# Kernel tuning notes

Measured on AMD Instinct MI355X. Metric: run time of the kernel, lower is better.

Reference implementation:

```python
import jax, jax.numpy as jnp
import numpy as np

N_NODES = 10000
D_IN = 128
D_OUT = 128
N_EDGES = 640000


def setup_inputs() -> dict:
    key = jax.random.key(0)
    k_x, k_e, k_wl, k_wr, k_b = jax.random.split(key, 5)
    x = jax.random.normal(k_x, (N_NODES, D_IN), dtype=jnp.float32)
    edge_index = jax.random.randint(k_e, (2, N_EDGES), 0, N_NODES, dtype=jnp.int64)
    # SAGEConv params: lin_l (neighbor path, with bias), lin_r (root path, no bias)
    s_l = 1.0 / np.sqrt(D_IN)
    W_l = jax.random.uniform(k_wl, (D_OUT, D_IN), dtype=jnp.float32, minval=-s_l, maxval=s_l)
    b_l = jax.random.uniform(k_b, (D_OUT,), dtype=jnp.float32, minval=-s_l, maxval=s_l)
    W_r = jax.random.uniform(k_wr, (D_OUT, D_IN), dtype=jnp.float32, minval=-s_l, maxval=s_l)
    return {"x": x, "edge_index": edge_index, "W_l": W_l, "b_l": b_l, "W_r": W_r}


def reference(x, edge_index, W_l, b_l, W_r):
    x = x.astype(jnp.float32)
    src, dst = edge_index[0], edge_index[1]
    # gather source features, mean-aggregate into destination nodes
    msgs = x[src]                                   # [E, D_in] irregular gather
    agg_sum = jax.ops.segment_sum(msgs, dst, num_segments=N_NODES)  # [N, D_in]
    deg = jax.ops.segment_sum(jnp.ones((src.shape[0],), dtype=x.dtype), dst,
                              num_segments=N_NODES)                 # [N]
    agg = jnp.where(deg[:, None] > 0, agg_sum / jnp.maximum(deg, 1.0)[:, None], 0.0)
    # SAGEConv: lin_l(agg) + lin_r(x)
    y = agg @ W_l.T + b_l + x @ W_r.T               # [N, D_out]
    return x + y                                     # residual add
```

## Files before the change

### kernel.cpp

```cpp
#include <hip/hip_runtime.h>

#define N_NODES 10000
#define D 128
#define N_EDGES 640000
#define NB 128
#define EPB (N_EDGES / NB)
#define SB 40
#define NPSB 250

typedef __attribute__((ext_vector_type(8))) short bf16x8;
typedef __attribute__((ext_vector_type(4))) float f32x4;
typedef __attribute__((ext_vector_type(8))) unsigned short us8;
typedef __attribute__((ext_vector_type(8))) float f32x8;


__device__ __forceinline__ unsigned short f2bf(float f) {
    union { float f; unsigned int i; } v;
    v.f = f;
    unsigned int b = v.i;
    unsigned int rounded = b + 0x7fffu + ((b >> 16) & 1u);
    return (unsigned short)(rounded >> 16);
}

__device__ __forceinline__ float bf2f(unsigned short u) {
    union { unsigned int i; float f; } v;
    v.i = ((unsigned int)u) << 16;
    return v.f;
}

__device__ __forceinline__ f32x8 bf2f8(us8 v) {
    f32x8 r;
#pragma unroll
    for (int t = 0; t < 8; ++t) r[t] = bf2f(v[t]);
    return r;
}


__global__ __launch_bounds__(1024) void hist_cast_kernel(const int* __restrict__ ei,
                                                         const float4* __restrict__ x4,
                                                         const float4* __restrict__ Wl4,
                                                         const float4* __restrict__ Wr4,
                                                         ushort4* __restrict__ xh4,
                                                         ushort4* __restrict__ Wlb4,
                                                         ushort4* __restrict__ Wrb4,
                                                         unsigned short* __restrict__ lrank,
                                                         unsigned short* __restrict__ cnt,
                                                         unsigned long long* __restrict__ flags) {
    __shared__ int h[N_NODES];
    for (int n = threadIdx.x; n < N_NODES; n += 1024) h[n] = 0;
    if (blockIdx.x == 0 && threadIdx.x < SB) flags[threadIdx.x] = 0ULL;

    const int gid = blockIdx.x * 1024 + threadIdx.x;
    for (int i = gid; i < N_NODES * D / 4; i += NB * 1024) {
        float4 v = x4[i];
        ushort4 o;
        o.x = f2bf(v.x); o.y = f2bf(v.y); o.z = f2bf(v.z); o.w = f2bf(v.w);
        xh4[i] = o;
    }
    if (gid < D * D / 4) {
        float4 a = Wl4[gid], b = Wr4[gid];
        ushort4 oa, ob;
        oa.x = f2bf(a.x); oa.y = f2bf(a.y); oa.z = f2bf(a.z); oa.w = f2bf(a.w);
        ob.x = f2bf(b.x); ob.y = f2bf(b.y); ob.z = f2bf(b.z); ob.w = f2bf(b.w);
        Wlb4[gid] = oa;
        Wrb4[gid] = ob;
    }
    __syncthreads();

    const int base = blockIdx.x * EPB;
    for (int e = base + threadIdx.x; e < base + EPB; e += 1024) {
        int d = ei[N_EDGES + e];
        lrank[e] = (unsigned short)atomicAdd(&h[d], 1);
    }
    __syncthreads();
    unsigned short* c = cnt + (size_t)blockIdx.x * N_NODES;
    for (int n = threadIdx.x; n < N_NODES; n += 1024) c[n] = (unsigned short)h[n];
}


__global__ __launch_bounds__(256) void colscan_scan_kernel(unsigned short* __restrict__ cnt,
                                                           int* __restrict__ row_start,
                                                           unsigned long long* __restrict__ flags) {
    const int t = threadIdx.x;
    const int b = blockIdx.x;
    const int n = b * NPSB + t;
    __shared__ int sc[256];
    __shared__ int blk_excl_sh;

    int deg = 0;
    if (t < NPSB) {
        int s = 0;
#pragma unroll 8
        for (int j = 0; j < NB; ++j) {
            int idx = j * N_NODES + n;
            int v = cnt[idx];
            cnt[idx] = (unsigned short)s;
            s += v;
        }
        deg = s;
    }
    sc[t] = deg;
    __syncthreads();
    for (int off = 1; off < 256; off <<= 1) {
        int v = (t >= off) ? sc[t - off] : 0;
        __syncthreads();
        sc[t] += v;
        __syncthreads();
    }
    const int total = sc[255];
    const int local_excl = sc[t] - deg;

    if (t == 0) {
        int excl = 0;
        if (b == 0) {
            __hip_atomic_store(&flags[0], (2ULL << 32) | (unsigned)total,
                               __ATOMIC_RELEASE, __HIP_MEMORY_SCOPE_AGENT);
        } else {
            __hip_atomic_store(&flags[b], (1ULL << 32) | (unsigned)total,
                               __ATOMIC_RELEASE, __HIP_MEMORY_SCOPE_AGENT);
            int j = b - 1;
            while (j >= 0) {
                unsigned long long f = __hip_atomic_load(&flags[j], __ATOMIC_ACQUIRE,
                                                         __HIP_MEMORY_SCOPE_AGENT);
                unsigned st = (unsigned)(f >> 32);
                if (st == 0) continue;
                excl += (int)(unsigned)(f & 0xffffffffULL);
                if (st == 2) break;
                --j;
            }
            __hip_atomic_store(&flags[b], (2ULL << 32) | (unsigned)(excl + total),
                               __ATOMIC_RELEASE, __HIP_MEMORY_SCOPE_AGENT);
        }
        blk_excl_sh = excl;
    }
    __syncthreads();
    if (t < NPSB) row_start[n] = blk_excl_sh + local_excl;
    if (b == SB - 1 && t == 0) row_start[N_NODES] = N_EDGES;
}

__global__ __launch_bounds__(256) void scatter_kernel(const int* __restrict__ ei,
                                                      const int* __restrict__ row_start,
                                                      const unsigned short* __restrict__ cnt,
                                                      const unsigned short* __restrict__ lrank,
                                                      unsigned short* __restrict__ csr) {
    int i = blockIdx.x * 256 + threadIdx.x;
    if (i < N_EDGES) {
        int b = i / EPB;
        int s = ei[i];
        int d = ei[N_EDGES + i];
        int pos = row_start[d] + (int)cnt[b * N_NODES + d] + (int)lrank[i];
        csr[pos] = (unsigned short)s;
    }
}


__global__ __launch_bounds__(128) void aggregate_kernel(const us8* __restrict__ xh8,
                                                        const int* __restrict__ row_start,
                                                        const unsigned short* __restrict__ csr,
                                                        us8* __restrict__ aggb8) {
    __shared__ unsigned short idxs[256];
    __shared__ f32x8 red[8][16];
    const int node = blockIdx.x;
    const int lane16 = threadIdx.x & 15;
    const int slot = threadIdx.x >> 4;
    const int start = row_start[node];
    const int end = row_start[node + 1];

    f32x8 a0 = 0.f, a1 = 0.f, a2 = 0.f, a3 = 0.f;
    for (int cs = start; cs < end; cs += 256) {
        int m = min(256, end - cs);
        if ((int)threadIdx.x < m) idxs[threadIdx.x] = csr[cs + threadIdx.x];
        if ((int)threadIdx.x + 128 < m) idxs[threadIdx.x + 128] = csr[cs + threadIdx.x + 128];
        __syncthreads();
        int j = slot;
        for (; j + 24 < m; j += 32) {
            int s0 = idxs[j], s1 = idxs[j + 8], s2 = idxs[j + 16], s3 = idxs[j + 24];
            us8 v0 = xh8[s0 * 16 + lane16];
            us8 v1 = xh8[s1 * 16 + lane16];
            us8 v2 = xh8[s2 * 16 + lane16];
            us8 v3 = xh8[s3 * 16 + lane16];
            a0 += bf2f8(v0); a1 += bf2f8(v1); a2 += bf2f8(v2); a3 += bf2f8(v3);
        }
        for (; j < m; j += 8) {
            us8 v = xh8[(int)idxs[j] * 16 + lane16];
            a0 += bf2f8(v);
        }
        __syncthreads();
    }
    a0 = (a0 + a1) + (a2 + a3);
    red[slot][lane16] = a0;
    __syncthreads();
    if (slot == 0) {
        f32x8 o = red[0][lane16];
#pragma unroll
        for (int s = 1; s < 8; ++s) o += red[s][lane16];
        int cntE = end - start;
        float inv = (cntE > 0) ? 1.0f / (float)cntE : 0.0f;
        us8 pack;
#pragma unroll
        for (int t = 0; t < 8; ++t) pack[t] = f2bf(o[t] * inv);
        aggb8[node * 16 + lane16] = pack;
    }
}


__global__ __launch_bounds__(256) void lin_mfma_kernel(const float* __restrict__ x,
                                                       const unsigned short* __restrict__ aggb,
                                                       const unsigned short* __restrict__ xh,
                                                       const unsigned short* __restrict__ Wlb,
                                                       const unsigned short* __restrict__ Wrb,
                                                       const float* __restrict__ bl,
                                                       float* __restrict__ out) {
    const int wave = threadIdx.x >> 6;
    const int lane = threadIdx.x & 63;
    const int l15 = lane & 15;
    const int quad = lane >> 4;
    const int mt = blockIdx.x * 4 + wave;
    if (mt >= 625) return;
    const int row0 = mt * 16;
    const int out0 = blockIdx.y * 16;

    const int m = row0 + l15;
    const int f = out0 + l15;

    const bf16x8* arow = (const bf16x8*)(aggb + (size_t)m * D) + quad;
    const bf16x8* xrow = (const bf16x8*)(xh   + (size_t)m * D) + quad;
    const bf16x8* wlro = (const bf16x8*)(Wlb + (size_t)f * D) + quad;
    const bf16x8* wrro = (const bf16x8*)(Wrb + (size_t)f * D) + quad;

    f32x4 c = {0.f, 0.f, 0.f, 0.f};
#pragma unroll
    for (int kk = 0; kk < 4; ++kk) {
        c = __builtin_amdgcn_mfma_f32_16x16x32_bf16(arow[kk * 4], wlro[kk * 4], c, 0, 0, 0);
        c = __builtin_amdgcn_mfma_f32_16x16x32_bf16(xrow[kk * 4], wrro[kk * 4], c, 0, 0, 0);
    }

    const float bias = bl[f];
#pragma unroll
    for (int r = 0; r < 4; ++r) {
        int row = row0 + quad * 4 + r;
        int idx = row * D + f;
        out[idx] = x[idx] + bias + c[r];
    }
}

extern "C" void kernel_launch(void* const* d_in, const int* in_sizes, int n_in,
                              void* d_out, int out_size, void* d_ws, size_t ws_size,
                              hipStream_t stream) {
    const float* x  = (const float*)d_in[0];
    const int*   ei = (const int*)d_in[1];
    const float* Wl = (const float*)d_in[2];
    const float* bl = (const float*)d_in[3];
    const float* Wr = (const float*)d_in[4];
    float* out = (float*)d_out;

    unsigned long long* flags = (unsigned long long*)d_ws;
    int* row_start = (int*)(flags + 64);
    unsigned short* cnt   = (unsigned short*)(row_start + 10016);
    unsigned short* lrank = cnt + (size_t)NB * N_NODES;
    unsigned short* csr   = lrank + N_EDGES;
    unsigned short* xh    = csr + N_EDGES;
    unsigned short* aggb  = xh + (size_t)N_NODES * D;
    unsigned short* Wlb   = aggb + (size_t)N_NODES * D;
    unsigned short* Wrb   = Wlb + D * D;

    hist_cast_kernel<<<NB, 1024, 0, stream>>>(ei, (const float4*)x, (const float4*)Wl,
                                              (const float4*)Wr, (ushort4*)xh,
                                              (ushort4*)Wlb, (ushort4*)Wrb,
                                              lrank, cnt, flags);
    colscan_scan_kernel<<<SB, 256, 0, stream>>>(cnt, row_start, flags);
    scatter_kernel<<<(N_EDGES + 255) / 256, 256, 0, stream>>>(ei, row_start, cnt, lrank, csr);
    aggregate_kernel<<<N_NODES, 128, 0, stream>>>((const us8*)xh, row_start, csr,
                                                  (us8*)aggb);
    lin_mfma_kernel<<<dim3(157, 8), 256, 0, stream>>>(x, aggb, xh, Wlb, Wrb, bl, out);
}
```

Measured before the change: 122.2 us.

## Replace per-block shared histograms with global atomic degree counting

Drops the 128 per-block shared-memory histograms and the column scan over the 128x10000 count matrix. Each edge now gets its rank from a global atomicAdd on a single degree array, which is zeroed with a memset. This removes the large count-matrix traffic and the serial 128-step column scan, and lets the cast/rank kernel run with more, smaller blocks. The cost is contention on global atomics (about 64 per node) and an extra memset launch. CSR order within a row becomes nondeterministic, which can change float summation order.

```diff
diff --git a/kernel.cpp b/kernel.cpp
--- a/kernel.cpp
+++ b/kernel.cpp
@@ -3,10 +3,9 @@
 #define N_NODES 10000
 #define D 128
 #define N_EDGES 640000
-#define NB 128
-#define EPB (N_EDGES / NB)
 #define SB 40
 #define NPSB 250
+#define RCB 640
 
 typedef __attribute__((ext_vector_type(8))) short bf16x8;
 typedef __attribute__((ext_vector_type(4))) float f32x4;
@@ -36,22 +35,17 @@
 }
 
 
-__global__ __launch_bounds__(1024) void hist_cast_kernel(const int* __restrict__ ei,
-                                                         const float4* __restrict__ x4,
-                                                         const float4* __restrict__ Wl4,
-                                                         const float4* __restrict__ Wr4,
-                                                         ushort4* __restrict__ xh4,
-                                                         ushort4* __restrict__ Wlb4,
-                                                         ushort4* __restrict__ Wrb4,
-                                                         unsigned short* __restrict__ lrank,
-                                                         unsigned short* __restrict__ cnt,
-                                                         unsigned long long* __restrict__ flags) {
-    __shared__ int h[N_NODES];
-    for (int n = threadIdx.x; n < N_NODES; n += 1024) h[n] = 0;
-    if (blockIdx.x == 0 && threadIdx.x < SB) flags[threadIdx.x] = 0ULL;
-
-    const int gid = blockIdx.x * 1024 + threadIdx.x;
-    for (int i = gid; i < N_NODES * D / 4; i += NB * 1024) {
+__global__ __launch_bounds__(256) void rank_cast_kernel(const int* __restrict__ ei,
+                                                        const float4* __restrict__ x4,
+                                                        const float4* __restrict__ Wl4,
+                                                        const float4* __restrict__ Wr4,
+                                                        ushort4* __restrict__ xh4,
+                                                        ushort4* __restrict__ Wlb4,
+                                                        ushort4* __restrict__ Wrb4,
+                                                        int* __restrict__ deg,
+                                                        unsigned short* __restrict__ lrank) {
+    const int gid = blockIdx.x * 256 + threadIdx.x;
+    for (int i = gid; i < N_NODES * D / 4; i += RCB * 256) {
         float4 v = x4[i];
         ushort4 o;
         o.x = f2bf(v.x); o.y = f2bf(v.y); o.z = f2bf(v.z); o.w = f2bf(v.w);
@@ -65,41 +59,25 @@
         Wlb4[gid] = oa;
         Wrb4[gid] = ob;
     }
-    __syncthreads();
-
-    const int base = blockIdx.x * EPB;
-    for (int e = base + threadIdx.x; e < base + EPB; e += 1024) {
+    for (int e = gid; e < N_EDGES; e += RCB * 256) {
         int d = ei[N_EDGES + e];
-        lrank[e] = (unsigned short)atomicAdd(&h[d], 1);
-    }
-    __syncthreads();
-    unsigned short* c = cnt + (size_t)blockIdx.x * N_NODES;
-    for (int n = threadIdx.x; n < N_NODES; n += 1024) c[n] = (unsigned short)h[n];
-}
-
-
-__global__ __launch_bounds__(256) void colscan_scan_kernel(unsigned short* __restrict__ cnt,
-                                                           int* __restrict__ row_start,
-                                                           unsigned long long* __restrict__ flags) {
+        lrank[e] = (unsigned short)atomicAdd(&deg[d], 1);
+    }
+}
+
+
+__global__ __launch_bounds__(256) void scan_kernel(const int* __restrict__ deg,
+                                                   int* __restrict__ row_start,
+                                                   unsigned long long* __restrict__ flags) {
     const int t = threadIdx.x;
     const int b = blockIdx.x;
     const int n = b * NPSB + t;
     __shared__ int sc[256];
     __shared__ int blk_excl_sh;
 
-    int deg = 0;
-    if (t < NPSB) {
-        int s = 0;
-#pragma unroll 8
-        for (int j = 0; j < NB; ++j) {
-            int idx = j * N_NODES + n;
-            int v = cnt[idx];
-            cnt[idx] = (unsigned short)s;
-            s += v;
-        }
-        deg = s;
-    }
-    sc[t] = deg;
+    int dv = 0;
+    if (t < NPSB) dv = deg[n];
+    sc[t] = dv;
     __syncthreads();
     for (int off = 1; off < 256; off <<= 1) {
         int v = (t >= off) ? sc[t - off] : 0;
@@ -108,7 +86,7 @@
         __syncthreads();
     }
     const int total = sc[255];
-    const int local_excl = sc[t] - deg;
+    const int local_excl = sc[t] - dv;
 
     if (t == 0) {
         int excl = 0;
@@ -138,18 +116,16 @@
     if (b == SB - 1 && t == 0) row_start[N_NODES] = N_EDGES;
 }
 
+
 __global__ __launch_bounds__(256) void scatter_kernel(const int* __restrict__ ei,
                                                       const int* __restrict__ row_start,
-                                                      const unsigned short* __restrict__ cnt,
                                                       const unsigned short* __restrict__ lrank,
                                                       unsigned short* __restrict__ csr) {
     int i = blockIdx.x * 256 + threadIdx.x;
     if (i < N_EDGES) {
-        int b = i / EPB;
         int s = ei[i];
         int d = ei[N_EDGES + i];
-        int pos = row_start[d] + (int)cnt[b * N_NODES + d] + (int)lrank[i];
-        csr[pos] = (unsigned short)s;
+        csr[row_start[d] + (int)lrank[i]] = (unsigned short)s;
     }
 }
 
@@ -255,21 +231,22 @@
     float* out = (float*)d_out;
 
     unsigned long long* flags = (unsigned long long*)d_ws;
-    int* row_start = (int*)(flags + 64);
-    unsigned short* cnt   = (unsigned short*)(row_start + 10016);
-    unsigned short* lrank = cnt + (size_t)NB * N_NODES;
+    int* deg = (int*)(flags + 64);
+    int* row_start = deg + 10016;
+    unsigned short* lrank = (unsigned short*)(row_start + 10016);
     unsigned short* csr   = lrank + N_EDGES;
     unsigned short* xh    = csr + N_EDGES;
     unsigned short* aggb  = xh + (size_t)N_NODES * D;
     unsigned short* Wlb   = aggb + (size_t)N_NODES * D;
     unsigned short* Wrb   = Wlb + D * D;
 
-    hist_cast_kernel<<<NB, 1024, 0, stream>>>(ei, (const float4*)x, (const float4*)Wl,
+    hipMemsetAsync(d_ws, 0, 512 + 10016 * 4, stream);
+
+    rank_cast_kernel<<<RCB, 256, 0, stream>>>(ei, (const float4*)x, (const float4*)Wl,
                                               (const float4*)Wr, (ushort4*)xh,
-                                              (ushort4*)Wlb, (ushort4*)Wrb,
-                                              lrank, cnt, flags);
-    colscan_scan_kernel<<<SB, 256, 0, stream>>>(cnt, row_start, flags);
-    scatter_kernel<<<(N_EDGES + 255) / 256, 256, 0, stream>>>(ei, row_start, cnt, lrank, csr);
+                                              (ushort4*)Wlb, (ushort4*)Wrb, deg, lrank);
+    scan_kernel<<<SB, 256, 0, stream>>>(deg, row_start, flags);
+    scatter_kernel<<<(N_EDGES + 255) / 256, 256, 0, stream>>>(ei, row_start, lrank, csr);
     aggregate_kernel<<<N_NODES, 128, 0, stream>>>((const us8*)xh, row_start, csr,
                                                   (us8*)aggb);
     lin_mfma_kernel<<<dim3(157, 8), 256, 0, stream>>>(x, aggb, xh, Wlb, Wrb, bl, out);
```

Result: slower. 147.8 us (+21.0%).

## Fuse neighbor aggregation and linear MFMA into one per-tile kernel

Applied to the files above, without the earlier changes.

Merges the per-node mean-aggregation kernel and the MFMA linear kernel into one kernel. Each 256-thread block aggregates 16 nodes one after another into a shared-memory bf16 tile, then runs the MFMA linear and residual add for that tile across all 128 output columns. This drops the global round trip of the bf16 aggregate buffer and one kernel launch. In exchange it cuts the grid from 10000 blocks to 625, processes nodes serially inside a block with extra barriers, and lowers parallelism for the gather-bound phase.

```diff
diff --git a/kernel.cpp b/kernel.cpp
--- a/kernel.cpp
+++ b/kernel.cpp
@@ -7,6 +7,7 @@
 #define EPB (N_EDGES / NB)
 #define SB 40
 #define NPSB 250
+#define NTILES 625
 
 typedef __attribute__((ext_vector_type(8))) short bf16x8;
 typedef __attribute__((ext_vector_type(4))) float f32x4;
@@ -138,6 +139,7 @@
     if (b == SB - 1 && t == 0) row_start[N_NODES] = N_EDGES;
 }
 
+
 __global__ __launch_bounds__(256) void scatter_kernel(const int* __restrict__ ei,
                                                       const int* __restrict__ row_start,
                                                       const unsigned short* __restrict__ cnt,
@@ -154,93 +156,93 @@
 }
 
 
-__global__ __launch_bounds__(128) void aggregate_kernel(const us8* __restrict__ xh8,
-                                                        const int* __restrict__ row_start,
-                                                        const unsigned short* __restrict__ csr,
-                                                        us8* __restrict__ aggb8) {
+__global__ __launch_bounds__(256) void agg_lin_kernel(const us8* __restrict__ xh8,
+                                                      const int* __restrict__ row_start,
+                                                      const unsigned short* __restrict__ csr,
+                                                      const float* __restrict__ x,
+                                                      const unsigned short* __restrict__ xh,
+                                                      const unsigned short* __restrict__ Wlb,
+                                                      const unsigned short* __restrict__ Wrb,
+                                                      const float* __restrict__ bl,
+                                                      float* __restrict__ out) {
     __shared__ unsigned short idxs[256];
-    __shared__ f32x8 red[8][16];
-    const int node = blockIdx.x;
-    const int lane16 = threadIdx.x & 15;
-    const int slot = threadIdx.x >> 4;
-    const int start = row_start[node];
-    const int end = row_start[node + 1];
-
-    f32x8 a0 = 0.f, a1 = 0.f, a2 = 0.f, a3 = 0.f;
-    for (int cs = start; cs < end; cs += 256) {
-        int m = min(256, end - cs);
-        if ((int)threadIdx.x < m) idxs[threadIdx.x] = csr[cs + threadIdx.x];
-        if ((int)threadIdx.x + 128 < m) idxs[threadIdx.x + 128] = csr[cs + threadIdx.x + 128];
-        __syncthreads();
-        int j = slot;
-        for (; j + 24 < m; j += 32) {
-            int s0 = idxs[j], s1 = idxs[j + 8], s2 = idxs[j + 16], s3 = idxs[j + 24];
-            us8 v0 = xh8[s0 * 16 + lane16];
-            us8 v1 = xh8[s1 * 16 + lane16];
-            us8 v2 = xh8[s2 * 16 + lane16];
-            us8 v3 = xh8[s3 * 16 + lane16];
-            a0 += bf2f8(v0); a1 += bf2f8(v1); a2 += bf2f8(v2); a3 += bf2f8(v3);
-        }
-        for (; j < m; j += 8) {
-            us8 v = xh8[(int)idxs[j] * 16 + lane16];
-            a0 += bf2f8(v);
-        }
-        __syncthreads();
-    }
-    a0 = (a0 + a1) + (a2 + a3);
-    red[slot][lane16] = a0;
-    __syncthreads();
-    if (slot == 0) {
-        f32x8 o = red[0][lane16];
-#pragma unroll
-        for (int s = 1; s < 8; ++s) o += red[s][lane16];
-        int cntE = end - start;
-        float inv = (cntE > 0) ? 1.0f / (float)cntE : 0.0f;
-        us8 pack;
-#pragma unroll
-        for (int t = 0; t < 8; ++t) pack[t] = f2bf(o[t] * inv);
-        aggb8[node * 16 + lane16] = pack;
-    }
-}
-
-
-__global__ __launch_bounds__(256) void lin_mfma_kernel(const float* __restrict__ x,
-                                                       const unsigned short* __restrict__ aggb,
-                                                       const unsigned short* __restrict__ xh,
-                                                       const unsigned short* __restrict__ Wlb,
-                                                       const unsigned short* __restrict__ Wrb,
-                                                       const float* __restrict__ bl,
-                                                       float* __restrict__ out) {
-    const int wave = threadIdx.x >> 6;
-    const int lane = threadIdx.x & 63;
+    __shared__ f32x8 red[16][16];
+    __shared__ unsigned short aggT[16][136];
+    const int tid = threadIdx.x;
+    const int lane16 = tid & 15;
+    const int slot = tid >> 4;
+    const int wave = tid >> 6;
+    const int lane = tid & 63;
+    const int quad = lane >> 4;
     const int l15 = lane & 15;
-    const int quad = lane >> 4;
-    const int mt = blockIdx.x * 4 + wave;
-    if (mt >= 625) return;
-    const int row0 = mt * 16;
-    const int out0 = blockIdx.y * 16;
-
-    const int m = row0 + l15;
-    const int f = out0 + l15;
-
-    const bf16x8* arow = (const bf16x8*)(aggb + (size_t)m * D) + quad;
-    const bf16x8* xrow = (const bf16x8*)(xh   + (size_t)m * D) + quad;
-    const bf16x8* wlro = (const bf16x8*)(Wlb + (size_t)f * D) + quad;
-    const bf16x8* wrro = (const bf16x8*)(Wrb + (size_t)f * D) + quad;
-
-    f32x4 c = {0.f, 0.f, 0.f, 0.f};
+    const int row0 = blockIdx.x * 16;
+
+    for (int nn = 0; nn < 16; ++nn) {
+        const int node = row0 + nn;
+        const int start = row_start[node];
+        const int end = row_start[node + 1];
+        f32x8 a0 = 0.f, a1 = 0.f, a2 = 0.f, a3 = 0.f;
+        for (int cs = start; cs < end; cs += 256) {
+            int m = min(256, end - cs);
+            __syncthreads();
+            if (tid < m) idxs[tid] = csr[cs + tid];
+            __syncthreads();
+            int j = slot;
+            for (; j + 48 < m; j += 64) {
+                int s0 = idxs[j], s1 = idxs[j + 16], s2 = idxs[j + 32], s3 = idxs[j + 48];
+                a0 += bf2f8(xh8[s0 * 16 + lane16]);
+                a1 += bf2f8(xh8[s1 * 16 + lane16]);
+                a2 += bf2f8(xh8[s2 * 16 + lane16]);
+                a3 += bf2f8(xh8[s3 * 16 + lane16]);
+            }
+            for (; j < m; j += 16) a0 += bf2f8(xh8[(int)idxs[j] * 16 + lane16]);
+        }
+        a0 = (a0 + a1) + (a2 + a3);
+        __syncthreads();
+        red[slot][lane16] = a0;
+        __syncthreads();
+        if (slot == 0) {
+            f32x8 o = red[0][lane16];
+#pragma unroll
+            for (int s2 = 1; s2 < 16; ++s2) o += red[s2][lane16];
+            int cE = end - start;
+            float inv = (cE > 0) ? 1.0f / (float)cE : 0.0f;
+            us8 pack;
+#pragma unroll
+            for (int t2 = 0; t2 < 8; ++t2) pack[t2] = f2bf(o[t2] * inv);
+            *(us8*)&aggT[nn][lane16 * 8] = pack;
+        }
+    }
+    __syncthreads();
+
+    const unsigned short* ap = &aggT[l15][quad * 8];
+    const bf16x8* xrow = (const bf16x8*)(xh + (size_t)(row0 + l15) * D) + quad;
+    const int f0 = wave * 32 + l15;
+    const int f1 = f0 + 16;
+    const bf16x8* wl0 = (const bf16x8*)(Wlb + (size_t)f0 * D) + quad;
+    const bf16x8* wr0 = (const bf16x8*)(Wrb + (size_t)f0 * D) + quad;
+    const bf16x8* wl1 = (const bf16x8*)(Wlb + (size_t)f1 * D) + quad;
+    const bf16x8* wr1 = (const bf16x8*)(Wrb + (size_t)f1 * D) + quad;
+    f32x4 c0 = {0.f, 0.f, 0.f, 0.f};
+    f32x4 c1 = {0.f, 0.f, 0.f, 0.f};
 #pragma unroll
     for (int kk = 0; kk < 4; ++kk) {
-        c = __builtin_amdgcn_mfma_f32_16x16x32_bf16(arow[kk * 4], wlro[kk * 4], c, 0, 0, 0);
-        c = __builtin_amdgcn_mfma_f32_16x16x32_bf16(xrow[kk * 4], wrro[kk * 4], c, 0, 0, 0);
-    }
-
-    const float bias = bl[f];
+        bf16x8 af = *(const bf16x8*)(ap + kk * 32);
+        bf16x8 xf = xrow[kk * 4];
+        c0 = __builtin_amdgcn_mfma_f32_16x16x32_bf16(af, wl0[kk * 4], c0, 0, 0, 0);
+        c0 = __builtin_amdgcn_mfma_f32_16x16x32_bf16(xf, wr0[kk * 4], c0, 0, 0, 0);
+        c1 = __builtin_amdgcn_mfma_f32_16x16x32_bf16(af, wl1[kk * 4], c1, 0, 0, 0);
+        c1 = __builtin_amdgcn_mfma_f32_16x16x32_bf16(xf, wr1[kk * 4], c1, 0, 0, 0);
+    }
+    const float b0 = bl[f0];
+    const float b1 = bl[f1];
 #pragma unroll
     for (int r = 0; r < 4; ++r) {
         int row = row0 + quad * 4 + r;
-        int idx = row * D + f;
-        out[idx] = x[idx] + bias + c[r];
+        int i0 = row * D + f0;
+        int i1 = row * D + f1;
+        out[i0] = x[i0] + b0 + c0[r];
+        out[i1] = x[i1] + b1 + c1[r];
     }
 }
 
@@ -260,8 +262,7 @@
     unsigned short* lrank = cnt + (size_t)NB * N_NODES;
     unsigned short* csr   = lrank + N_EDGES;
     unsigned short* xh    = csr + N_EDGES;
-    unsigned short* aggb  = xh + (size_t)N_NODES * D;
-    unsigned short* Wlb   = aggb + (size_t)N_NODES * D;
+    unsigned short* Wlb   = xh + (size_t)N_NODES * D;
     unsigned short* Wrb   = Wlb + D * D;
 
     hist_cast_kernel<<<NB, 1024, 0, stream>>>(ei, (const float4*)x, (const float4*)Wl,
@@ -270,7 +271,6 @@
                                               lrank, cnt, flags);
     colscan_scan_kernel<<<SB, 256, 0, stream>>>(cnt, row_start, flags);
     scatter_kernel<<<(N_EDGES + 255) / 256, 256, 0, stream>>>(ei, row_start, cnt, lrank, csr);
-    aggregate_kernel<<<N_NODES, 128, 0, stream>>>((const us8*)xh, row_start, csr,
-                                                  (us8*)aggb);
-    lin_mfma_kernel<<<dim3(157, 8), 256, 0, stream>>>(x, aggb, xh, Wlb, Wrb, bl, out);
-}
+    agg_lin_kernel<<<NTILES, 256, 0, stream>>>((const us8*)xh, row_start, csr,
+                                               x, xh, Wlb, Wrb, bl, out);
+}
```

New measurement: 136.5 us. 11.7% more time.
